# Kernel tuning notes

Measured on AMD Instinct MI355X. Metric: run time of the kernel, lower is better.

The kernel has to match this reference:

```python
import jax, jax.numpy as jnp
import numpy as np

B, N = 2048, 64
D, H = 64, 256
CARD_V, UNIT_V, ENEMY_V, AT_V, SRC_V, MODE_V, TER_V, SITE_V, SKILL_V = 400, 100, 120, 50, 30, 10, 12, 25, 60
STATE_SC, CE_SC, SITE_SC, ME_SC, ACT_SC = 64, 8, 6, 8, 16
L_HAND, L_UNIT, L_CE, L_SK, L_VS, L_ME, L_TGT = 16, 8, 8, 8, 16, 16, 8
STATE_IN = STATE_SC + 6 * D + (D + CE_SC) + (D + SITE_SC) + (D + ME_SC)  # 662
ACT_IN = 7 * D + ACT_SC  # 464


def setup_inputs() -> dict:
    key = jax.random.key(0)
    ks = iter(jax.random.split(key, 64))
    nrm = lambda shape, s=1.0: jax.random.normal(next(ks), shape, jnp.float32) * s
    ri = lambda shape, hi: jax.random.randint(next(ks), shape, 0, hi, jnp.int32)
    return {
        'state_scalars': nrm((B, STATE_SC)),
        'mode_id': ri((B,), MODE_V), 'terrain_id': ri((B,), TER_V), 'site_type_id': ri((B,), SITE_V),
        'hand_ids': ri((B, L_HAND), CARD_V), 'hand_mask': ri((B, L_HAND), 2),
        'unit_ids': ri((B, L_UNIT), UNIT_V), 'unit_mask': ri((B, L_UNIT), 2),
        'combat_enemy_ids': ri((B, L_CE), ENEMY_V), 'combat_enemy_scalars': nrm((B, L_CE, CE_SC)), 'combat_enemy_mask': ri((B, L_CE), 2),
        'skill_ids': ri((B, L_SK), SKILL_V), 'skill_mask': ri((B, L_SK), 2),
        'visible_site_ids': ri((B, L_VS), SITE_V), 'visible_site_scalars': nrm((B, L_VS, SITE_SC)), 'visible_site_mask': ri((B, L_VS), 2),
        'map_enemy_ids': ri((B, L_ME), ENEMY_V), 'map_enemy_scalars': nrm((B, L_ME, ME_SC)), 'map_enemy_mask': ri((B, L_ME), 2),
        'action_ids': ri((B, N, 6), SRC_V),  # SRC_V=30 is min over the 6 id vocabs -> always in range
        'action_scalars': nrm((B, N, ACT_SC)),
        'target_enemy_ids': ri((B, N, L_TGT), ENEMY_V), 'target_mask': ri((B, N, L_TGT), 2),
        'card_emb': nrm((CARD_V, D), 0.05), 'unit_emb': nrm((UNIT_V, D), 0.05), 'enemy_emb': nrm((ENEMY_V, D), 0.05),
        'action_type_emb': nrm((AT_V, D), 0.05), 'source_emb': nrm((SRC_V, D), 0.05), 'mode_emb': nrm((MODE_V, D), 0.05),
        'terrain_emb': nrm((TER_V, D), 0.05), 'site_emb': nrm((SITE_V, D), 0.05), 'skill_emb': nrm((SKILL_V, D), 0.05),
        'map_site_emb': nrm((SITE_V, D), 0.05),
        'W_s': nrm((STATE_IN, H), 0.02), 'b_s': jnp.zeros((H,), jnp.float32),
        'W_a': nrm((ACT_IN, H), 0.02), 'b_a': jnp.zeros((H,), jnp.float32),
        'W1': nrm((2 * H, H), 0.02), 'b1': jnp.zeros((H,), jnp.float32),
        'W2': nrm((H, 1), 0.02), 'b2': jnp.zeros((1,), jnp.float32),
        'W_v': nrm((H, 1), 0.02), 'b_v': jnp.zeros((1,), jnp.float32),
    }


def masked_mean(x, mask):
    # x: [..., L, D'], mask: [..., L] (0/1). Empty list -> zeros (count clamped to 1).
    m = mask.astype(x.dtype)[..., None]
    s = jnp.sum(x * m, axis=-2)
    c = jnp.maximum(jnp.sum(m, axis=-2), 1.0)
    return s / c


def reference(state_scalars, mode_id, terrain_id, site_type_id, hand_ids, hand_mask,
              unit_ids, unit_mask, combat_enemy_ids, combat_enemy_scalars, combat_enemy_mask,
              skill_ids, skill_mask, visible_site_ids, visible_site_scalars, visible_site_mask,
              map_enemy_ids, map_enemy_scalars, map_enemy_mask, action_ids, action_scalars,
              target_enemy_ids, target_mask, card_emb, unit_emb, enemy_emb, action_type_emb,
              source_emb, mode_emb, terrain_emb, site_emb, skill_emb, map_site_emb,
              W_s, b_s, W_a, b_a, W1, b1, W2, b2, W_v, b_v):
    # ---- state encoding (batched version of encode_state) ----
    hand_pool = masked_mean(card_emb[hand_ids], hand_mask)            # [B, D]
    unit_pool = masked_mean(unit_emb[unit_ids], unit_mask)            # [B, D]
    ce = jnp.concatenate([enemy_emb[combat_enemy_ids], combat_enemy_scalars], axis=-1)
    ce_pool = masked_mean(ce, combat_enemy_mask)                      # [B, D+CE_SC]
    skill_pool = masked_mean(skill_emb[skill_ids], skill_mask)        # [B, D]
    vs = jnp.concatenate([map_site_emb[visible_site_ids], visible_site_scalars], axis=-1)
    vs_pool = masked_mean(vs, visible_site_mask)                      # [B, D+SITE_SC]
    me = jnp.concatenate([enemy_emb[map_enemy_ids], map_enemy_scalars], axis=-1)
    me_pool = masked_mean(me, map_enemy_mask)                         # [B, D+ME_SC]
    state_input = jnp.concatenate([
        state_scalars, mode_emb[mode_id], hand_pool, unit_pool,
        terrain_emb[terrain_id], site_emb[site_type_id],
        ce_pool, skill_pool, vs_pool, me_pool], axis=-1)              # [B, 662]
    state_repr = jnp.tanh(state_input @ W_s + b_s)                    # [B, H]
    # ---- action encoding (batched encode_actions) ----
    tgt_pool = masked_mean(enemy_emb[target_enemy_ids], target_mask)  # [B, N, D]
    action_input = jnp.concatenate([
        action_type_emb[action_ids[..., 0]], source_emb[action_ids[..., 1]],
        card_emb[action_ids[..., 2]], unit_emb[action_ids[..., 3]],
        enemy_emb[action_ids[..., 4]], skill_emb[action_ids[..., 5]],
        tgt_pool, action_scalars], axis=-1)                           # [B, N, 464]
    action_reprs = jnp.tanh(action_input @ W_a + b_a)                 # [B, N, H]
    # ---- scoring + value heads ----
    state_b = jnp.broadcast_to(state_repr[:, None, :], (state_repr.shape[0], action_reprs.shape[1], state_repr.shape[1]))
    combined = jnp.concatenate([state_b, action_reprs], axis=-1)      # [B, N, 2H]
    logits = (jnp.tanh(combined @ W1 + b1) @ W2 + b2)[..., 0]         # [B, N]
    value = (state_repr @ W_v + b_v)[..., 0]                          # [B]
    return logits, value
```

## Files before the change

### kernel.cpp

```cpp
#include <hip/hip_runtime.h>
#include <hip/hip_bf16.h>

#define BB 2048
#define NN 64
#define DD 64
#define HH 256
#define L_HAND 16
#define L_UNIT 8
#define L_CE 8
#define L_SK 8
#define L_VS 16
#define L_ME 16
#define L_TGT 8
#define STATE_SC 64
#define CE_SC 8
#define SITE_SC 6
#define ME_SC 8
#define ACT_SC 16
#define STATE_IN 662
#define ACT_IN 464

#define SROWS 2
#define SK 672
#define SSTRIDE 676

typedef __attribute__((ext_vector_type(8))) short short8;
typedef __attribute__((ext_vector_type(4))) float f32x4;

__device__ __forceinline__ float fast_tanh(float x) {
    float e = __expf(2.0f * x);
    return 1.0f - 2.0f * __builtin_amdgcn_rcpf(e + 1.0f);
}
__device__ __forceinline__ short f2bs(float x) {
    __hip_bfloat16 h = __float2bfloat16(x);
    return *reinterpret_cast<short*>(&h);
}
__device__ __forceinline__ float bs2f(short u) {
    union { unsigned int i; float f; } v;
    v.i = ((unsigned int)(unsigned short)u) << 16;
    return v.f;
}
__device__ __forceinline__ void async_copy16(const void* gsrc, void* ldst) {
    __builtin_amdgcn_global_load_lds(
        (const __attribute__((address_space(1))) unsigned int*)gsrc,
        (__attribute__((address_space(3))) unsigned int*)ldst, 16, 0, 0);
}
__device__ __forceinline__ float sum16_dpp(float v) {
    int x;
    x = __builtin_amdgcn_update_dpp(0, __float_as_int(v), 0x111, 0xf, 0xf, true);
    v += __int_as_float(x);
    x = __builtin_amdgcn_update_dpp(0, __float_as_int(v), 0x112, 0xf, 0xf, true);
    v += __int_as_float(x);
    x = __builtin_amdgcn_update_dpp(0, __float_as_int(v), 0x114, 0xf, 0xf, true);
    v += __int_as_float(x);
    x = __builtin_amdgcn_update_dpp(0, __float_as_int(v), 0x118, 0xf, 0xf, true);
    v += __int_as_float(x);
    return v;
}

#define RO_AT    0
#define RO_SRC   50
#define RO_CARD  80
#define RO_UNIT  480
#define RO_ENEMY 580
#define RO_SKILL 700
#define EMB_ROWS 760

#define T0 (480 * 256)
#define T1 (T0 + 256 * 256)
#define T2 (T1 + EMB_ROWS * 64)
#define T3 (T2 + SK * 256)
#define T4 (T3 + 256 * 256)

__global__ __launch_bounds__(256) void pack_kernel(
    const float* __restrict__ W_a, const float* __restrict__ W1,
    const float* __restrict__ W_s,
    const float* __restrict__ at_emb, const float* __restrict__ src_emb,
    const float* __restrict__ card_emb, const float* __restrict__ unit_emb,
    const float* __restrict__ enemy_emb, const float* __restrict__ skill_emb,
    ushort* __restrict__ WaP, ushort* __restrict__ W1bP, ushort* __restrict__ emb16,
    ushort* __restrict__ WsP, ushort* __restrict__ W1aP)
{
    const int idx = blockIdx.x * 256 + threadIdx.x;
    if (idx < T0) {
        const int k = idx >> 8, n = idx & 255;
        const float v = (k < ACT_IN) ? W_a[k * HH + n] : 0.f;
        const int pi = (((k >> 5) * 16 + (n >> 4)) * 64 +
                        ((n & 15) + 16 * ((k >> 3) & 3))) * 8 + (k & 7);
        WaP[pi] = (ushort)f2bs(v);
    } else if (idx < T1) {
        const int j = idx - T0;
        const int k = j >> 8, n = j & 255;
        const float v = W1[(256 + k) * HH + n];
        const int pi = (((k >> 5) * 16 + (n >> 4)) * 64 +
                        ((n & 15) + 16 * ((k >> 3) & 3))) * 8 + (k & 7);
        W1bP[pi] = (ushort)f2bs(v);
    } else if (idx < T2) {
        const int j = idx - T1;
        const int row = j >> 6, d = j & 63;
        float v;
        if      (row < RO_SRC)   v = at_emb[row * 64 + d];
        else if (row < RO_CARD)  v = src_emb[(row - RO_SRC) * 64 + d];
        else if (row < RO_UNIT)  v = card_emb[(row - RO_CARD) * 64 + d];
        else if (row < RO_ENEMY) v = unit_emb[(row - RO_UNIT) * 64 + d];
        else if (row < RO_SKILL) v = enemy_emb[(row - RO_ENEMY) * 64 + d];
        else                     v = skill_emb[(row - RO_SKILL) * 64 + d];
        emb16[j] = (ushort)f2bs(v);
    } else if (idx < T3) {
        const int j = idx - T2;
        const int k = j >> 8, n = j & 255;
        const float v = (k < STATE_IN) ? W_s[k * HH + n] : 0.f;
        const int pi = (((k >> 5) * 16 + (n >> 4)) * 64 +
                        ((n & 15) + 16 * ((k >> 3) & 3))) * 8 + (k & 7);
        WsP[pi] = (ushort)f2bs(v);
    } else if (idx < T4) {
        const int j = idx - T3;
        const int k = j >> 8, n = j & 255;
        const float v = W1[k * HH + n];
        const int pi = (((k >> 5) * 16 + (n >> 4)) * 64 +
                        ((n & 15) + 16 * ((k >> 3) & 3))) * 8 + (k & 7);
        W1aP[pi] = (ushort)f2bs(v);
    }
}

__global__ __launch_bounds__(256) void state_mfma_kernel(
    const float* __restrict__ state_scalars,
    const int* __restrict__ mode_id, const int* __restrict__ terrain_id,
    const int* __restrict__ site_type_id,
    const int* __restrict__ hand_ids, const int* __restrict__ hand_mask,
    const int* __restrict__ unit_ids, const int* __restrict__ unit_mask,
    const int* __restrict__ ce_ids, const float* __restrict__ ce_sc, const int* __restrict__ ce_mask,
    const int* __restrict__ skill_ids, const int* __restrict__ skill_mask,
    const int* __restrict__ vs_ids, const float* __restrict__ vs_sc, const int* __restrict__ vs_mask,
    const int* __restrict__ me_ids, const float* __restrict__ me_sc, const int* __restrict__ me_mask,
    const float* __restrict__ mode_emb, const float* __restrict__ ter_emb,
    const float* __restrict__ site_emb, const float* __restrict__ msite_emb,
    const ushort* __restrict__ emb16,
    const ushort* __restrict__ WsP, const float* __restrict__ b_s,
    const ushort* __restrict__ W1aP,
    const float* __restrict__ W_v, const float* __restrict__ b_v,
    float* __restrict__ s_part, float* __restrict__ out_value)
{
    __shared__ float s_in[SROWS * SSTRIDE];
    __shared__ ushort sA2[8 * 64 * 8];
    __shared__ float red[4][4];

    const int t = threadIdx.x;
    const int b0 = blockIdx.x * SROWS;
    const int w = t >> 6;
    const int lane = t & 63;
    const ushort* card16  = emb16 + RO_CARD  * 64;
    const ushort* unit16  = emb16 + RO_UNIT  * 64;
    const ushort* enemy16 = emb16 + RO_ENEMY * 64;
    const ushort* skill16 = emb16 + RO_SKILL * 64;

    for (int u = t; u < SROWS * 84; u += 256) {
        const int r  = u / 84;
        const int un = u - r * 84;
        const int b  = b0 + r;
        float* dst = s_in + r * SSTRIDE;
        if (un < 8) {
            const int o0 = un * 8;
            const float4 f0 = *(const float4*)(state_scalars + b * STATE_SC + o0);
            const float4 f1 = *(const float4*)(state_scalars + b * STATE_SC + o0 + 4);
            *(float4*)(dst + o0) = f0; *(float4*)(dst + o0 + 4) = f1;
        } else if (un < 16) {
            const int d0 = (un - 8) * 8;
            const float4 f0 = *(const float4*)(mode_emb + mode_id[b] * DD + d0);
            const float4 f1 = *(const float4*)(mode_emb + mode_id[b] * DD + d0 + 4);
            *(float4*)(dst + 64 + d0) = f0; *(float4*)(dst + 64 + d0 + 4) = f1;
        } else if (un < 24) {
            const int d0 = (un - 16) * 8;
            float acc[8] = {0,0,0,0,0,0,0,0}; int c = 0;
#pragma unroll
            for (int l = 0; l < L_HAND; ++l) {
                const int mk = hand_mask[b * L_HAND + l]; c += mk;
                const float fm = (float)mk;
                const short8 e = *(const short8*)(card16 + hand_ids[b * L_HAND + l] * 64 + d0);
#pragma unroll
                for (int q = 0; q < 8; ++q) acc[q] = fmaf(fm, bs2f(e[q]), acc[q]);
            }
            const float inv = 1.0f / (float)(c > 1 ? c : 1);
#pragma unroll
            for (int q = 0; q < 8; ++q) dst[128 + d0 + q] = acc[q] * inv;
        } else if (un < 32) {
            const int d0 = (un - 24) * 8;
            float acc[8] = {0,0,0,0,0,0,0,0}; int c = 0;
#pragma unroll
            for (int l = 0; l < L_UNIT; ++l) {
                const int mk = unit_mask[b * L_UNIT + l]; c += mk;
                const float fm = (float)mk;
                const short8 e = *(const short8*)(unit16 + unit_ids[b * L_UNIT + l] * 64 + d0);
#pragma unroll
                for (int q = 0; q < 8; ++q) acc[q] = fmaf(fm, bs2f(e[q]), acc[q]);
            }
            const float inv = 1.0f / (float)(c > 1 ? c : 1);
#pragma unroll
            for (int q = 0; q < 8; ++q) dst[192 + d0 + q] = acc[q] * inv;
        } else if (un < 40) {
            const int d0 = (un - 32) * 8;
            const float4 f0 = *(const float4*)(ter_emb + terrain_id[b] * DD + d0);
            const float4 f1 = *(const float4*)(ter_emb + terrain_id[b] * DD + d0 + 4);
            *(float4*)(dst + 256 + d0) = f0; *(float4*)(dst + 256 + d0 + 4) = f1;
        } else if (un < 48) {
            const int d0 = (un - 40) * 8;
            const float4 f0 = *(const float4*)(site_emb + site_type_id[b] * DD + d0);
            const float4 f1 = *(const float4*)(site_emb + site_type_id[b] * DD + d0 + 4);
            *(float4*)(dst + 320 + d0) = f0; *(float4*)(dst + 320 + d0 + 4) = f1;
        } else if (un < 56) {
            const int d0 = (un - 48) * 8;
            float acc[8] = {0,0,0,0,0,0,0,0}; int c = 0;
#pragma unroll
            for (int l = 0; l < L_CE; ++l) {
                const int mk = ce_mask[b * L_CE + l]; c += mk;
                const float fm = (float)mk;
                const short8 e = *(const short8*)(enemy16 + ce_ids[b * L_CE + l] * 64 + d0);
#pragma unroll
                for (int q = 0; q < 8; ++q) acc[q] = fmaf(fm, bs2f(e[q]), acc[q]);
            }
            const float inv = 1.0f / (float)(c > 1 ? c : 1);
#pragma unroll
            for (int q = 0; q < 8; ++q) dst[384 + d0 + q] = acc[q] * inv;
        } else if (un == 56) {
            float acc[8] = {0,0,0,0,0,0,0,0}; int c = 0;
#pragma unroll
            for (int l = 0; l < L_CE; ++l) {
                const int mk = ce_mask[b * L_CE + l]; c += mk;
                const float fm = (float)mk;
                const float4 f0 = *(const float4*)(ce_sc + (b * L_CE + l) * CE_SC);
                const float4 f1 = *(const float4*)(ce_sc + (b * L_CE + l) * CE_SC + 4);
                acc[0] = fmaf(fm, f0.x, acc[0]); acc[1] = fmaf(fm, f0.y, acc[1]);
                acc[2] = fmaf(fm, f0.z, acc[2]); acc[3] = fmaf(fm, f0.w, acc[3]);
                acc[4] = fmaf(fm, f1.x, acc[4]); acc[5] = fmaf(fm, f1.y, acc[5]);
                acc[6] = fmaf(fm, f1.z, acc[6]); acc[7] = fmaf(fm, f1.w, acc[7]);
            }
            const float inv = 1.0f / (float)(c > 1 ? c : 1);
#pragma unroll
            for (int q = 0; q < 8; ++q) dst[448 + q] = acc[q] * inv;
        } else if (un < 65) {
            const int d0 = (un - 57) * 8;
            float acc[8] = {0,0,0,0,0,0,0,0}; int c = 0;
#pragma unroll
            for (int l = 0; l < L_SK; ++l) {
                const int mk = skill_mask[b * L_SK + l]; c += mk;
                const float fm = (float)mk;
                const short8 e = *(const short8*)(skill16 + skill_ids[b * L_SK + l] * 64 + d0);
#pragma unroll
                for (int q = 0; q < 8; ++q) acc[q] = fmaf(fm, bs2f(e[q]), acc[q]);
            }
            const float inv = 1.0f / (float)(c > 1 ? c : 1);
#pragma unroll
            for (int q = 0; q < 8; ++q) dst[456 + d0 + q] = acc[q] * inv;
        } else if (un < 73) {
            const int d0 = (un - 65) * 8;
            float acc[8] = {0,0,0,0,0,0,0,0}; int c = 0;
#pragma unroll
            for (int l = 0; l < L_VS; ++l) {
                const int mk = vs_mask[b * L_VS + l]; c += mk;
                const float fm = (float)mk;
                const float4 f0 = *(const float4*)(msite_emb + vs_ids[b * L_VS + l] * DD + d0);
                const float4 f1 = *(const float4*)(msite_emb + vs_ids[b * L_VS + l] * DD + d0 + 4);
                acc[0] = fmaf(fm, f0.x, acc[0]); acc[1] = fmaf(fm, f0.y, acc[1]);
                acc[2] = fmaf(fm, f0.z, acc[2]); acc[3] = fmaf(fm, f0.w, acc[3]);
                acc[4] = fmaf(fm, f1.x, acc[4]); acc[5] = fmaf(fm, f1.y, acc[5]);
                acc[6] = fmaf(fm, f1.z, acc[6]); acc[7] = fmaf(fm, f1.w, acc[7]);
            }
            const float inv = 1.0f / (float)(c > 1 ? c : 1);
#pragma unroll
            for (int q = 0; q < 8; ++q) dst[520 + d0 + q] = acc[q] * inv;
        } else if (un == 73) {
            float acc[6] = {0,0,0,0,0,0}; int c = 0;
#pragma unroll
            for (int l = 0; l < L_VS; ++l) {
                const int mk = vs_mask[b * L_VS + l]; c += mk;
                const float fm = (float)mk;
                const float* p = vs_sc + (b * L_VS + l) * SITE_SC;
#pragma unroll
                for (int q = 0; q < 6; ++q) acc[q] = fmaf(fm, p[q], acc[q]);
            }
            const float inv = 1.0f / (float)(c > 1 ? c : 1);
#pragma unroll
            for (int q = 0; q < 6; ++q) dst[584 + q] = acc[q] * inv;
        } else if (un < 82) {
            const int d0 = (un - 74) * 8;
            float acc[8] = {0,0,0,0,0,0,0,0}; int c = 0;
#pragma unroll
            for (int l = 0; l < L_ME; ++l) {
                const int mk = me_mask[b * L_ME + l]; c += mk;
                const float fm = (float)mk;
                const short8 e = *(const short8*)(enemy16 + me_ids[b * L_ME + l] * 64 + d0);
#pragma unroll
                for (int q = 0; q < 8; ++q) acc[q] = fmaf(fm, bs2f(e[q]), acc[q]);
            }
            const float inv = 1.0f / (float)(c > 1 ? c : 1);
#pragma unroll
            for (int q = 0; q < 8; ++q) dst[590 + d0 + q] = acc[q] * inv;
        } else if (un == 82) {
            float acc[8] = {0,0,0,0,0,0,0,0}; int c = 0;
#pragma unroll
            for (int l = 0; l < L_ME; ++l) {
                const int mk = me_mask[b * L_ME + l]; c += mk;
                const float fm = (float)mk;
                const float4 f0 = *(const float4*)(me_sc + (b * L_ME + l) * ME_SC);
                const float4 f1 = *(const float4*)(me_sc + (b * L_ME + l) * ME_SC + 4);
                acc[0] = fmaf(fm, f0.x, acc[0]); acc[1] = fmaf(fm, f0.y, acc[1]);
                acc[2] = fmaf(fm, f0.z, acc[2]); acc[3] = fmaf(fm, f0.w, acc[3]);
                acc[4] = fmaf(fm, f1.x, acc[4]); acc[5] = fmaf(fm, f1.y, acc[5]);
                acc[6] = fmaf(fm, f1.z, acc[6]); acc[7] = fmaf(fm, f1.w, acc[7]);
            }
            const float inv = 1.0f / (float)(c > 1 ? c : 1);
#pragma unroll
            for (int q = 0; q < 8; ++q) dst[654 + q] = acc[q] * inv;
        } else {
#pragma unroll
            for (int q = 0; q < 10; ++q) dst[662 + q] = 0.f;
        }
    }
    __syncthreads();

    const short8* Ws8  = (const short8*)WsP;
    const short8* W1a8 = (const short8*)W1aP;
    const f32x4 zero = {0.f, 0.f, 0.f, 0.f};
    const int m15 = lane & 15;
    const int g = lane >> 4;
    const float* arow = s_in + (m15 & (SROWS - 1)) * SSTRIDE;

    f32x4 acc1[4];
#pragma unroll
    for (int nt = 0; nt < 4; ++nt) acc1[nt] = zero;

    for (int kt = 0; kt < 21; ++kt) {
        const int k0 = kt * 32 + 8 * g;
        const float4 v0 = *(const float4*)(arow + k0);
        const float4 v1 = *(const float4*)(arow + k0 + 4);
        short8 a;
        a[0] = f2bs(v0.x); a[1] = f2bs(v0.y); a[2] = f2bs(v0.z); a[3] = f2bs(v0.w);
        a[4] = f2bs(v1.x); a[5] = f2bs(v1.y); a[6] = f2bs(v1.z); a[7] = f2bs(v1.w);
        short8 bfr[4];
#pragma unroll
        for (int nt = 0; nt < 4; ++nt) bfr[nt] = Ws8[(kt * 16 + w * 4 + nt) * 64 + lane];
#pragma unroll
        for (int nt = 0; nt < 4; ++nt)
            acc1[nt] = __builtin_amdgcn_mfma_f32_16x16x32_bf16(a, bfr[nt], acc1[nt], 0, 0, 0);
    }

    float sr[4][4];
    float pv[4] = {0.f, 0.f, 0.f, 0.f};
#pragma unroll
    for (int nt = 0; nt < 4; ++nt) {
        const int n = w * 64 + nt * 16 + m15;
        const float bsn = b_s[n];
        const float wvn = W_v[n];
#pragma unroll
        for (int r = 0; r < 4; ++r) {
            const float sv = fast_tanh(acc1[nt][r] + bsn);
            sr[nt][r] = sv;
            pv[r] = fmaf(sv, wvn, pv[r]);
        }
    }
#pragma unroll
    for (int r = 0; r < SROWS; ++r) {
        float v = pv[r];
        v += __shfl_xor(v, 1);
        v += __shfl_xor(v, 2);
        v += __shfl_xor(v, 4);
        v += __shfl_xor(v, 8);
        if (lane == 0) red[w][r] = v;
    }
    if (g == 0) {
#pragma unroll
        for (int nt = 0; nt < 4; ++nt) {
            const int n = w * 64 + nt * 16 + m15;
            const int kt2 = n >> 5;
            const int lo16 = (n >> 3) & 3;
#pragma unroll
            for (int r = 0; r < 4; ++r) {
                const int pi = (kt2 * 64 + (r + 16 * lo16)) * 8 + (n & 7);
                sA2[pi] = (ushort)f2bs(sr[nt][r]);
            }
        }
    }
    __syncthreads();

    if (t < SROWS) {
        out_value[b0 + t] = red[0][t] + red[1][t] + red[2][t] + red[3][t] + b_v[0];
    }

    const short8* sA2_8 = (const short8*)sA2;
    f32x4 acc2[4];
#pragma unroll
    for (int nt = 0; nt < 4; ++nt) acc2[nt] = zero;
#pragma unroll
    for (int kt = 0; kt < 8; ++kt) {
        const short8 a2 = sA2_8[kt * 64 + lane];
        short8 bfr[4];
#pragma unroll
        for (int nt = 0; nt < 4; ++nt) bfr[nt] = W1a8[(kt * 16 + w * 4 + nt) * 64 + lane];
#pragma unroll
        for (int nt = 0; nt < 4; ++nt)
            acc2[nt] = __builtin_amdgcn_mfma_f32_16x16x32_bf16(a2, bfr[nt], acc2[nt], 0, 0, 0);
    }
    if (g == 0) {
#pragma unroll
        for (int nt = 0; nt < 4; ++nt) {
            const int n = w * 64 + nt * 16 + m15;
#pragma unroll
            for (int r = 0; r < SROWS; ++r)
                s_part[(b0 + r) * HH + n] = acc2[nt][r];
        }
    }
}

__device__ __forceinline__ short8 tail_chunk(
    int k0, int m, int b,
    const int* __restrict__ tgt_ids, const int* __restrict__ tgt_mask,
    const ushort* __restrict__ emb16, const float* __restrict__ action_scalars)
{
    short8 val;
    if (k0 < 448) {
        const int d = k0 - 384;
        const ushort* enemy16 = emb16 + RO_ENEMY * 64;
        const int base = (b * NN + m) * L_TGT;
        const int4 t0v = *(const int4*)(tgt_ids + base);
        const int4 t1v = *(const int4*)(tgt_ids + base + 4);
        const int4 m0v = *(const int4*)(tgt_mask + base);
        const int4 m1v = *(const int4*)(tgt_mask + base + 4);
        const int tid[8] = {t0v.x, t0v.y, t0v.z, t0v.w, t1v.x, t1v.y, t1v.z, t1v.w};
        const int tmk[8] = {m0v.x, m0v.y, m0v.z, m0v.w, m1v.x, m1v.y, m1v.z, m1v.w};
        float accq[8] = {0.f, 0.f, 0.f, 0.f, 0.f, 0.f, 0.f, 0.f};
        int c = 0;
#pragma unroll
        for (int l = 0; l < L_TGT; ++l) {
            const int mk = tmk[l];
            c += mk;
            const float fm = (float)mk;
            const short8 e = *(const short8*)(enemy16 + tid[l] * 64 + d);
#pragma unroll
            for (int q = 0; q < 8; ++q) accq[q] = fmaf(fm, bs2f(e[q]), accq[q]);
        }
        const float inv = 1.0f / (float)(c > 1 ? c : 1);
#pragma unroll
        for (int q = 0; q < 8; ++q) val[q] = f2bs(accq[q] * inv);
    } else if (k0 < 464) {
        const float* sc = action_scalars + (b * NN + m) * ACT_SC + (k0 - 448);
        const float4 f0 = *(const float4*)sc;
        const float4 f1 = *(const float4*)(sc + 4);
        val[0] = f2bs(f0.x); val[1] = f2bs(f0.y); val[2] = f2bs(f0.z); val[3] = f2bs(f0.w);
        val[4] = f2bs(f1.x); val[5] = f2bs(f1.y); val[6] = f2bs(f1.z); val[7] = f2bs(f1.w);
    } else {
#pragma unroll
        for (int q = 0; q < 8; ++q) val[q] = 0;
    }
    return val;
}

__global__ __launch_bounds__(512) void action_mfma_kernel(
    const int* __restrict__ action_ids, const float* __restrict__ action_scalars,
    const int* __restrict__ tgt_ids, const int* __restrict__ tgt_mask,
    const ushort* __restrict__ emb16,
    const ushort* __restrict__ WaP, const float* __restrict__ b_a,
    const ushort* __restrict__ W1bP, const float* __restrict__ b1,
    const float* __restrict__ W2, const float* __restrict__ b2,
    const float* __restrict__ s_part, float* __restrict__ out_logits)
{
    __shared__ ushort sA[15 * 2048];
    __shared__ float red[8][64];

    const int t = threadIdx.x;
    const int b = blockIdx.x;
    const int w = t >> 6;
    const int lane = t & 63;
    const int m15 = lane & 15;

    const short8* sA8  = (const short8*)sA;
    short8* sA8w = (short8*)sA;
    const short8* Wa8  = (const short8*)WaP;
    const short8* W1b8 = (const short8*)W1bP;
    const f32x4 zero = {0.f, 0.f, 0.f, 0.f};
    const int* aid = action_ids + b * (NN * 6);

    short8 bp00 = Wa8[(0 * 16 + w * 2 + 0) * 64 + lane];
    short8 bp01 = Wa8[(0 * 16 + w * 2 + 1) * 64 + lane];
    short8 bp10 = Wa8[(1 * 16 + w * 2 + 0) * 64 + lane];
    short8 bp11 = Wa8[(1 * 16 + w * 2 + 1) * 64 + lane];

    const int ROFFS[6] = {RO_AT, RO_SRC, RO_CARD, RO_UNIT, RO_ENEMY, RO_SKILL};

    {
        const int kt = w;
        const int j = kt >> 1;
        const int roff = ROFFS[j];
        const int koff = (kt & 1) * 32 + (lane >> 4) * 8;
#pragma unroll
        for (int i = 0; i < 4; ++i) {
            const int id = aid[(i * 16 + m15) * 6 + j];
            async_copy16(emb16 + (roff + id) * 64 + koff, sA + kt * 2048 + i * 512);
        }
    }
    if (w < 4) {
        const int kt = 8 + w;
        const int j = kt >> 1;
        const int roff = ROFFS[j];
        const int koff = (kt & 1) * 32 + (lane >> 4) * 8;
#pragma unroll
        for (int i = 0; i < 4; ++i) {
            const int id = aid[(i * 16 + m15) * 6 + j];
            async_copy16(emb16 + (roff + id) * 64 + koff, sA + kt * 2048 + i * 512);
        }
    }

    {
        const int m = lane;
        const int mt_b = m >> 4, mrow = m & 15;
        for (int kc = 48 + w; kc < 60; kc += 8) {
            const int k0 = kc << 3;
            const short8 val = tail_chunk(k0, m, b, tgt_ids, tgt_mask, emb16, action_scalars);
            const int ktl = k0 >> 5;
            const int lo = kc & 3;
            sA8w[(ktl * 4 + mt_b) * 64 + mrow + 16 * lo] = val;
        }
    }
    __syncthreads();

    float ba[2];
#pragma unroll
    for (int nt = 0; nt < 2; ++nt) ba[nt] = b_a[w * 32 + nt * 16 + m15];

    f32x4 acc[4][2];
#pragma unroll
    for (int i = 0; i < 4; ++i) { acc[i][0] = zero; acc[i][1] = zero; }

#pragma unroll
    for (int kt = 0; kt < 15; ++kt) {
        short8 b0, b1;
        if ((kt & 1) == 0) { b0 = bp00; b1 = bp01; }
        else               { b0 = bp10; b1 = bp11; }
        if (kt + 2 < 15) {
            if ((kt & 1) == 0) {
                bp00 = Wa8[((kt + 2) * 16 + w * 2 + 0) * 64 + lane];
                bp01 = Wa8[((kt + 2) * 16 + w * 2 + 1) * 64 + lane];
            } else {
                bp10 = Wa8[((kt + 2) * 16 + w * 2 + 0) * 64 + lane];
                bp11 = Wa8[((kt + 2) * 16 + w * 2 + 1) * 64 + lane];
            }
        } else if (kt + 2 == 15) {
            bp10 = W1b8[(0 * 16 + w * 2 + 0) * 64 + lane];
            bp11 = W1b8[(0 * 16 + w * 2 + 1) * 64 + lane];
        } else {
            bp00 = W1b8[(1 * 16 + w * 2 + 0) * 64 + lane];
            bp01 = W1b8[(1 * 16 + w * 2 + 1) * 64 + lane];
        }
        short8 a[4];
#pragma unroll
        for (int mti = 0; mti < 4; ++mti) a[mti] = sA8[(kt * 4 + mti) * 64 + lane];
#pragma unroll
        for (int mti = 0; mti < 4; ++mti) {
            acc[mti][0] = __builtin_amdgcn_mfma_f32_16x16x32_bf16(a[mti], b0, acc[mti][0], 0, 0, 0);
            acc[mti][1] = __builtin_amdgcn_mfma_f32_16x16x32_bf16(a[mti], b1, acc[mti][1], 0, 0, 0);
        }
    }
    __syncthreads();

#pragma unroll
    for (int mti = 0; mti < 4; ++mti)
#pragma unroll
        for (int nt = 0; nt < 2; ++nt) {
            const int n = w * 32 + nt * 16 + m15;
            const int kt2 = n >> 5;
            const int lo16 = (n >> 3) & 3;
#pragma unroll
            for (int r = 0; r < 4; ++r) {
                const int mm = mti * 16 + (lane >> 4) * 4 + r;
                const float h = fast_tanh(acc[mti][nt][r] + ba[nt]);
                const int pi = ((kt2 * 4 + mti) * 64 + ((mm & 15) + 16 * lo16)) * 8 + (n & 7);
                sA[pi] = (ushort)f2bs(h);
            }
        }
    __syncthreads();

    float sp[2], w2v[2];
#pragma unroll
    for (int nt = 0; nt < 2; ++nt) {
        const int n = w * 32 + nt * 16 + m15;
        sp[nt]  = s_part[b * HH + n] + b1[n];
        w2v[nt] = W2[n];
    }

#pragma unroll
    for (int i = 0; i < 4; ++i) { acc[i][0] = zero; acc[i][1] = zero; }

#pragma unroll
    for (int kt = 0; kt < 8; ++kt) {
        short8 b0, b1;
        if ((kt & 1) == 0) { b0 = bp10; b1 = bp11; }
        else               { b0 = bp00; b1 = bp01; }
        if (kt + 2 < 8) {
            if ((kt & 1) == 0) {
                bp10 = W1b8[((kt + 2) * 16 + w * 2 + 0) * 64 + lane];
                bp11 = W1b8[((kt + 2) * 16 + w * 2 + 1) * 64 + lane];
            } else {
                bp00 = W1b8[((kt + 2) * 16 + w * 2 + 0) * 64 + lane];
                bp01 = W1b8[((kt + 2) * 16 + w * 2 + 1) * 64 + lane];
            }
        }
        short8 a[4];
#pragma unroll
        for (int mti = 0; mti < 4; ++mti) a[mti] = sA8[(kt * 4 + mti) * 64 + lane];
#pragma unroll
        for (int mti = 0; mti < 4; ++mti) {
            acc[mti][0] = __builtin_amdgcn_mfma_f32_16x16x32_bf16(a[mti], b0, acc[mti][0], 0, 0, 0);
            acc[mti][1] = __builtin_amdgcn_mfma_f32_16x16x32_bf16(a[mti], b1, acc[mti][1], 0, 0, 0);
        }
    }

    float part[4][4];
#pragma unroll
    for (int mti = 0; mti < 4; ++mti)
#pragma unroll
        for (int r = 0; r < 4; ++r) part[mti][r] = 0.f;

#pragma unroll
    for (int mti = 0; mti < 4; ++mti)
#pragma unroll
        for (int nt = 0; nt < 2; ++nt)
#pragma unroll
            for (int r = 0; r < 4; ++r)
                part[mti][r] += fast_tanh(acc[mti][nt][r] + sp[nt]) * w2v[nt];

#pragma unroll
    for (int mti = 0; mti < 4; ++mti)
#pragma unroll
        for (int r = 0; r < 4; ++r)
            part[mti][r] = sum16_dpp(part[mti][r]);

    if (m15 == 15) {
#pragma unroll
        for (int mti = 0; mti < 4; ++mti)
#pragma unroll
            for (int r = 0; r < 4; ++r) {
                const int mm = mti * 16 + (lane >> 4) * 4 + r;
                red[w][mm] = part[mti][r];
            }
    }
    __syncthreads();
    if (t < 64) {
        float s = b2[0];
#pragma unroll
        for (int wi = 0; wi < 8; ++wi) s += red[wi][t];
        out_logits[b * NN + t] = s;
    }
}

extern "C" void kernel_launch(void* const* d_in, const int* in_sizes, int n_in,
                              void* d_out, int out_size, void* d_ws, size_t ws_size,
                              hipStream_t stream) {
    const float* state_scalars = (const float*)d_in[0];
    const int*   mode_id       = (const int*)d_in[1];
    const int*   terrain_id    = (const int*)d_in[2];
    const int*   site_type_id  = (const int*)d_in[3];
    const int*   hand_ids      = (const int*)d_in[4];
    const int*   hand_mask     = (const int*)d_in[5];
    const int*   unit_ids      = (const int*)d_in[6];
    const int*   unit_mask     = (const int*)d_in[7];
    const int*   ce_ids        = (const int*)d_in[8];
    const float* ce_sc         = (const float*)d_in[9];
    const int*   ce_mask       = (const int*)d_in[10];
    const int*   skill_ids     = (const int*)d_in[11];
    const int*   skill_mask    = (const int*)d_in[12];
    const int*   vs_ids        = (const int*)d_in[13];
    const float* vs_sc         = (const float*)d_in[14];
    const int*   vs_mask       = (const int*)d_in[15];
    const int*   me_ids        = (const int*)d_in[16];
    const float* me_sc         = (const float*)d_in[17];
    const int*   me_mask       = (const int*)d_in[18];
    const int*   action_ids    = (const int*)d_in[19];
    const float* action_scalars= (const float*)d_in[20];
    const int*   tgt_ids       = (const int*)d_in[21];
    const int*   tgt_mask      = (const int*)d_in[22];
    const float* card_emb      = (const float*)d_in[23];
    const float* unit_emb      = (const float*)d_in[24];
    const float* enemy_emb     = (const float*)d_in[25];
    const float* at_emb        = (const float*)d_in[26];
    const float* src_emb       = (const float*)d_in[27];
    const float* mode_emb      = (const float*)d_in[28];
    const float* ter_emb       = (const float*)d_in[29];
    const float* site_emb      = (const float*)d_in[30];
    const float* skill_emb     = (const float*)d_in[31];
    const float* msite_emb     = (const float*)d_in[32];
    const float* W_s           = (const float*)d_in[33];
    const float* b_s           = (const float*)d_in[34];
    const float* W_a           = (const float*)d_in[35];
    const float* b_a           = (const float*)d_in[36];
    const float* W1            = (const float*)d_in[37];
    const float* b1            = (const float*)d_in[38];
    const float* W2            = (const float*)d_in[39];
    const float* b2            = (const float*)d_in[40];
    const float* W_v           = (const float*)d_in[41];
    const float* b_v           = (const float*)d_in[42];

    float* out_logits = (float*)d_out;
    float* out_value  = (float*)d_out + (size_t)BB * NN;

    char* ws = (char*)d_ws;
    float*  s_part = (float*)ws;
    ushort* WaP    = (ushort*)(ws + 2097152);
    ushort* W1bP   = (ushort*)(ws + 2342912);
    ushort* emb16  = (ushort*)(ws + 2473984);
    ushort* WsP    = (ushort*)(ws + 2571264);
    ushort* W1aP   = (ushort*)(ws + 2915328);

    pack_kernel<<<(T4 + 255) / 256, 256, 0, stream>>>(
        W_a, W1, W_s, at_emb, src_emb, card_emb, unit_emb, enemy_emb, skill_emb,
        WaP, W1bP, emb16, WsP, W1aP);

    state_mfma_kernel<<<BB / SROWS, 256, 0, stream>>>(
        state_scalars, mode_id, terrain_id, site_type_id,
        hand_ids, hand_mask, unit_ids, unit_mask,
        ce_ids, ce_sc, ce_mask, skill_ids, skill_mask,
        vs_ids, vs_sc, vs_mask, me_ids, me_sc, me_mask,
        mode_emb, ter_emb, site_emb, msite_emb, emb16,
        WsP, b_s, W1aP, W_v, b_v, s_part, out_value);

    action_mfma_kernel<<<BB, 512, 0, stream>>>(
        action_ids, action_scalars, tgt_ids, tgt_mask,
        emb16, WaP, b_a, W1bP, b1, W2, b2, s_part, out_logits);
}
```

Baseline: 111.0 us.

## Make action kernel persistent over batch rows with double-buffered async staging

Each block of the action kernel now processes 8 batch rows instead of one, and launches BB/8 blocks. While row i is being computed, the embedding gather and tail staging for row i+1 go into a second LDS buffer via async global-to-LDS copies. Weight prefetch depth grows from 2 to 4 k-tiles, and barriers become explicit waitcnt plus s_barrier. This should hide gather latency and amortise per-block setup, but it doubles LDS use, which can cut occupancy. Only 256 blocks are launched, so CU utilisation may also drop.

New measurement: 137.3 us. 1.24x slower.

```diff
diff --git a/kernel.cpp b/kernel.cpp
--- a/kernel.cpp
+++ b/kernel.cpp
@@ -23,6 +23,7 @@
 #define SROWS 2
 #define SK 672
 #define SSTRIDE 676
+#define RPB 8
 
 typedef __attribute__((ext_vector_type(8))) short short8;
 typedef __attribute__((ext_vector_type(4))) float f32x4;
@@ -57,6 +58,12 @@
     v += __int_as_float(x);
     return v;
 }
+
+#define LGKM0()  asm volatile("s_waitcnt lgkmcnt(0)" ::: "memory")
+#define VMLG0()  asm volatile("s_waitcnt vmcnt(0) lgkmcnt(0)" ::: "memory")
+#define RAWBAR() do { __builtin_amdgcn_sched_barrier(0); \
+                      __builtin_amdgcn_s_barrier();       \
+                      __builtin_amdgcn_sched_barrier(0); } while (0)
 
 #define RO_AT    0
 #define RO_SRC   50
@@ -463,191 +470,192 @@
     const float* __restrict__ W2, const float* __restrict__ b2,
     const float* __restrict__ s_part, float* __restrict__ out_logits)
 {
-    __shared__ ushort sA[15 * 2048];
+    __shared__ ushort sA[2][15 * 2048];
     __shared__ float red[8][64];
 
     const int t = threadIdx.x;
-    const int b = blockIdx.x;
     const int w = t >> 6;
     const int lane = t & 63;
     const int m15 = lane & 15;
-
-    const short8* sA8  = (const short8*)sA;
-    short8* sA8w = (short8*)sA;
+    const int b_base = blockIdx.x * RPB;
+
     const short8* Wa8  = (const short8*)WaP;
     const short8* W1b8 = (const short8*)W1bP;
     const f32x4 zero = {0.f, 0.f, 0.f, 0.f};
-    const int* aid = action_ids + b * (NN * 6);
-
-    short8 bp00 = Wa8[(0 * 16 + w * 2 + 0) * 64 + lane];
-    short8 bp01 = Wa8[(0 * 16 + w * 2 + 1) * 64 + lane];
-    short8 bp10 = Wa8[(1 * 16 + w * 2 + 0) * 64 + lane];
-    short8 bp11 = Wa8[(1 * 16 + w * 2 + 1) * 64 + lane];
-
     const int ROFFS[6] = {RO_AT, RO_SRC, RO_CARD, RO_UNIT, RO_ENEMY, RO_SKILL};
 
-    {
-        const int kt = w;
-        const int j = kt >> 1;
-        const int roff = ROFFS[j];
-        const int koff = (kt & 1) * 32 + (lane >> 4) * 8;
-#pragma unroll
-        for (int i = 0; i < 4; ++i) {
-            const int id = aid[(i * 16 + m15) * 6 + j];
-            async_copy16(emb16 + (roff + id) * 64 + koff, sA + kt * 2048 + i * 512);
-        }
-    }
-    if (w < 4) {
-        const int kt = 8 + w;
-        const int j = kt >> 1;
-        const int roff = ROFFS[j];
-        const int koff = (kt & 1) * 32 + (lane >> 4) * 8;
-#pragma unroll
-        for (int i = 0; i < 4; ++i) {
-            const int id = aid[(i * 16 + m15) * 6 + j];
-            async_copy16(emb16 + (roff + id) * 64 + koff, sA + kt * 2048 + i * 512);
-        }
-    }
-
-    {
-        const int m = lane;
-        const int mt_b = m >> 4, mrow = m & 15;
+    float ba[2], w2v[2], b1v[2];
+#pragma unroll
+    for (int nt = 0; nt < 2; ++nt) {
+        const int n = w * 32 + nt * 16 + m15;
+        ba[nt]  = b_a[n];
+        w2v[nt] = W2[n];
+        b1v[nt] = b1[n];
+    }
+    const float b2v = b2[0];
+
+    auto STAGE = [&](int b, ushort* sbuf) {
+        const int* aid = action_ids + b * (NN * 6);
+        {
+            const int kt = w;
+            const int j = kt >> 1;
+            const int roff = ROFFS[j];
+            const int koff = (kt & 1) * 32 + (lane >> 4) * 8;
+#pragma unroll
+            for (int i = 0; i < 4; ++i) {
+                const int id = aid[(i * 16 + m15) * 6 + j];
+                async_copy16(emb16 + (roff + id) * 64 + koff, sbuf + kt * 2048 + i * 512);
+            }
+        }
+        if (w < 4) {
+            const int kt = 8 + w;
+            const int j = kt >> 1;
+            const int roff = ROFFS[j];
+            const int koff = (kt & 1) * 32 + (lane >> 4) * 8;
+#pragma unroll
+            for (int i = 0; i < 4; ++i) {
+                const int id = aid[(i * 16 + m15) * 6 + j];
+                async_copy16(emb16 + (roff + id) * 64 + koff, sbuf + kt * 2048 + i * 512);
+            }
+        }
+        short8* s8 = (short8*)sbuf;
+        const int m = lane, mt_b = m >> 4, mrow = m & 15;
         for (int kc = 48 + w; kc < 60; kc += 8) {
             const int k0 = kc << 3;
             const short8 val = tail_chunk(k0, m, b, tgt_ids, tgt_mask, emb16, action_scalars);
-            const int ktl = k0 >> 5;
-            const int lo = kc & 3;
-            sA8w[(ktl * 4 + mt_b) * 64 + mrow + 16 * lo] = val;
-        }
-    }
-    __syncthreads();
-
-    float ba[2];
-#pragma unroll
-    for (int nt = 0; nt < 2; ++nt) ba[nt] = b_a[w * 32 + nt * 16 + m15];
-
-    f32x4 acc[4][2];
-#pragma unroll
-    for (int i = 0; i < 4; ++i) { acc[i][0] = zero; acc[i][1] = zero; }
-
-#pragma unroll
-    for (int kt = 0; kt < 15; ++kt) {
-        short8 b0, b1;
-        if ((kt & 1) == 0) { b0 = bp00; b1 = bp01; }
-        else               { b0 = bp10; b1 = bp11; }
-        if (kt + 2 < 15) {
-            if ((kt & 1) == 0) {
-                bp00 = Wa8[((kt + 2) * 16 + w * 2 + 0) * 64 + lane];
-                bp01 = Wa8[((kt + 2) * 16 + w * 2 + 1) * 64 + lane];
+            s8[((k0 >> 5) * 4 + mt_b) * 64 + mrow + 16 * (kc & 3)] = val;
+        }
+    };
+
+    STAGE(b_base, &sA[0][0]);
+    VMLG0();
+    RAWBAR();
+
+    for (int i = 0; i < RPB; ++i) {
+        const int b = b_base + i;
+        const short8* cur = (const short8*)&sA[i & 1][0];
+        ushort* curw = &sA[i & 1][0];
+
+        if (i + 1 < RPB) STAGE(b + 1, &sA[(i + 1) & 1][0]);
+
+        short8 bq[4][2];
+#pragma unroll
+        for (int p = 0; p < 4; ++p) {
+            bq[p][0] = Wa8[(p * 16 + w * 2 + 0) * 64 + lane];
+            bq[p][1] = Wa8[(p * 16 + w * 2 + 1) * 64 + lane];
+        }
+
+        f32x4 acc[4][2];
+#pragma unroll
+        for (int x = 0; x < 4; ++x) { acc[x][0] = zero; acc[x][1] = zero; }
+
+#pragma unroll
+        for (int kt = 0; kt < 15; ++kt) {
+            const int s = kt & 3;
+            const short8 bf0 = bq[s][0], bf1 = bq[s][1];
+            if (kt + 4 < 15) {
+                bq[s][0] = Wa8[((kt + 4) * 16 + w * 2 + 0) * 64 + lane];
+                bq[s][1] = Wa8[((kt + 4) * 16 + w * 2 + 1) * 64 + lane];
             } else {
-                bp10 = Wa8[((kt + 2) * 16 + w * 2 + 0) * 64 + lane];
-                bp11 = Wa8[((kt + 2) * 16 + w * 2 + 1) * 64 + lane];
-            }
-        } else if (kt + 2 == 15) {
-            bp10 = W1b8[(0 * 16 + w * 2 + 0) * 64 + lane];
-            bp11 = W1b8[(0 * 16 + w * 2 + 1) * 64 + lane];
-        } else {
-            bp00 = W1b8[(1 * 16 + w * 2 + 0) * 64 + lane];
-            bp01 = W1b8[(1 * 16 + w * 2 + 1) * 64 + lane];
-        }
-        short8 a[4];
-#pragma unroll
-        for (int mti = 0; mti < 4; ++mti) a[mti] = sA8[(kt * 4 + mti) * 64 + lane];
-#pragma unroll
-        for (int mti = 0; mti < 4; ++mti) {
-            acc[mti][0] = __builtin_amdgcn_mfma_f32_16x16x32_bf16(a[mti], b0, acc[mti][0], 0, 0, 0);
-            acc[mti][1] = __builtin_amdgcn_mfma_f32_16x16x32_bf16(a[mti], b1, acc[mti][1], 0, 0, 0);
-        }
-    }
-    __syncthreads();
-
-#pragma unroll
-    for (int mti = 0; mti < 4; ++mti)
-#pragma unroll
-        for (int nt = 0; nt < 2; ++nt) {
-            const int n = w * 32 + nt * 16 + m15;
-            const int kt2 = n >> 5;
-            const int lo16 = (n >> 3) & 3;
-#pragma unroll
-            for (int r = 0; r < 4; ++r) {
-                const int mm = mti * 16 + (lane >> 4) * 4 + r;
-                const float h = fast_tanh(acc[mti][nt][r] + ba[nt]);
-                const int pi = ((kt2 * 4 + mti) * 64 + ((mm & 15) + 16 * lo16)) * 8 + (n & 7);
-                sA[pi] = (ushort)f2bs(h);
-            }
-        }
-    __syncthreads();
-
-    float sp[2], w2v[2];
-#pragma unroll
-    for (int nt = 0; nt < 2; ++nt) {
-        const int n = w * 32 + nt * 16 + m15;
-        sp[nt]  = s_part[b * HH + n] + b1[n];
-        w2v[nt] = W2[n];
-    }
-
-#pragma unroll
-    for (int i = 0; i < 4; ++i) { acc[i][0] = zero; acc[i][1] = zero; }
-
-#pragma unroll
-    for (int kt = 0; kt < 8; ++kt) {
-        short8 b0, b1;
-        if ((kt & 1) == 0) { b0 = bp10; b1 = bp11; }
-        else               { b0 = bp00; b1 = bp01; }
-        if (kt + 2 < 8) {
-            if ((kt & 1) == 0) {
-                bp10 = W1b8[((kt + 2) * 16 + w * 2 + 0) * 64 + lane];
-                bp11 = W1b8[((kt + 2) * 16 + w * 2 + 1) * 64 + lane];
-            } else {
-                bp00 = W1b8[((kt + 2) * 16 + w * 2 + 0) * 64 + lane];
-                bp01 = W1b8[((kt + 2) * 16 + w * 2 + 1) * 64 + lane];
-            }
-        }
-        short8 a[4];
-#pragma unroll
-        for (int mti = 0; mti < 4; ++mti) a[mti] = sA8[(kt * 4 + mti) * 64 + lane];
-#pragma unroll
-        for (int mti = 0; mti < 4; ++mti) {
-            acc[mti][0] = __builtin_amdgcn_mfma_f32_16x16x32_bf16(a[mti], b0, acc[mti][0], 0, 0, 0);
-            acc[mti][1] = __builtin_amdgcn_mfma_f32_16x16x32_bf16(a[mti], b1, acc[mti][1], 0, 0, 0);
-        }
-    }
-
-    float part[4][4];
-#pragma unroll
-    for (int mti = 0; mti < 4; ++mti)
-#pragma unroll
-        for (int r = 0; r < 4; ++r) part[mti][r] = 0.f;
-
-#pragma unroll
-    for (int mti = 0; mti < 4; ++mti)
+                const int g2 = kt - 11;
+                bq[s][0] = W1b8[(g2 * 16 + w * 2 + 0) * 64 + lane];
+                bq[s][1] = W1b8[(g2 * 16 + w * 2 + 1) * 64 + lane];
+            }
+            short8 a[4];
+#pragma unroll
+            for (int mti = 0; mti < 4; ++mti) a[mti] = cur[(kt * 4 + mti) * 64 + lane];
+#pragma unroll
+            for (int mti = 0; mti < 4; ++mti) {
+                acc[mti][0] = __builtin_amdgcn_mfma_f32_16x16x32_bf16(a[mti], bf0, acc[mti][0], 0, 0, 0);
+                acc[mti][1] = __builtin_amdgcn_mfma_f32_16x16x32_bf16(a[mti], bf1, acc[mti][1], 0, 0, 0);
+            }
+        }
+        LGKM0();
+        RAWBAR();
+
+#pragma unroll
+        for (int mti = 0; mti < 4; ++mti)
+#pragma unroll
+            for (int nt = 0; nt < 2; ++nt) {
+                const int n = w * 32 + nt * 16 + m15;
+                const int kt2 = n >> 5;
+                const int lo16 = (n >> 3) & 3;
+#pragma unroll
+                for (int r = 0; r < 4; ++r) {
+                    const int mm = mti * 16 + (lane >> 4) * 4 + r;
+                    const float h = fast_tanh(acc[mti][nt][r] + ba[nt]);
+                    const int pi = ((kt2 * 4 + mti) * 64 + ((mm & 15) + 16 * lo16)) * 8 + (n & 7);
+                    curw[pi] = (ushort)f2bs(h);
+                }
+            }
+        float sp[2];
 #pragma unroll
         for (int nt = 0; nt < 2; ++nt)
+            sp[nt] = s_part[b * HH + (w * 32 + nt * 16 + m15)] + b1v[nt];
+
+        LGKM0();
+        RAWBAR();
+
+#pragma unroll
+        for (int x = 0; x < 4; ++x) { acc[x][0] = zero; acc[x][1] = zero; }
+
+#pragma unroll
+        for (int kt = 0; kt < 8; ++kt) {
+            const int s = (kt + 3) & 3;
+            const short8 bf0 = bq[s][0], bf1 = bq[s][1];
+            if (kt + 4 < 8) {
+                bq[s][0] = W1b8[((kt + 4) * 16 + w * 2 + 0) * 64 + lane];
+                bq[s][1] = W1b8[((kt + 4) * 16 + w * 2 + 1) * 64 + lane];
+            }
+            short8 a[4];
+#pragma unroll
+            for (int mti = 0; mti < 4; ++mti) a[mti] = cur[(kt * 4 + mti) * 64 + lane];
+#pragma unroll
+            for (int mti = 0; mti < 4; ++mti) {
+                acc[mti][0] = __builtin_amdgcn_mfma_f32_16x16x32_bf16(a[mti], bf0, acc[mti][0], 0, 0, 0);
+                acc[mti][1] = __builtin_amdgcn_mfma_f32_16x16x32_bf16(a[mti], bf1, acc[mti][1], 0, 0, 0);
+            }
+        }
+
+        float part[4][4];
+#pragma unroll
+        for (int mti = 0; mti < 4; ++mti)
+#pragma unroll
+            for (int r = 0; r < 4; ++r) part[mti][r] = 0.f;
+
+#pragma unroll
+        for (int mti = 0; mti < 4; ++mti)
+#pragma unroll
+            for (int nt = 0; nt < 2; ++nt)
+#pragma unroll
+                for (int r = 0; r < 4; ++r)
+                    part[mti][r] += fast_tanh(acc[mti][nt][r] + sp[nt]) * w2v[nt];
+
+#pragma unroll
+        for (int mti = 0; mti < 4; ++mti)
 #pragma unroll
             for (int r = 0; r < 4; ++r)
-                part[mti][r] += fast_tanh(acc[mti][nt][r] + sp[nt]) * w2v[nt];
-
-#pragma unroll
-    for (int mti = 0; mti < 4; ++mti)
-#pragma unroll
-        for (int r = 0; r < 4; ++r)
-            part[mti][r] = sum16_dpp(part[mti][r]);
-
-    if (m15 == 15) {
-#pragma unroll
-        for (int mti = 0; mti < 4; ++mti)
-#pragma unroll
-            for (int r = 0; r < 4; ++r) {
-                const int mm = mti * 16 + (lane >> 4) * 4 + r;
-                red[w][mm] = part[mti][r];
-            }
-    }
-    __syncthreads();
-    if (t < 64) {
-        float s = b2[0];
-#pragma unroll
-        for (int wi = 0; wi < 8; ++wi) s += red[wi][t];
-        out_logits[b * NN + t] = s;
+                part[mti][r] = sum16_dpp(part[mti][r]);
+
+        if (m15 == 15) {
+#pragma unroll
+            for (int mti = 0; mti < 4; ++mti)
+#pragma unroll
+                for (int r = 0; r < 4; ++r) {
+                    const int mm = mti * 16 + (lane >> 4) * 4 + r;
+                    red[w][mm] = part[mti][r];
+                }
+        }
+
+        VMLG0();
+        RAWBAR();
+
+        if (t < 64) {
+            float s = b2v;
+#pragma unroll
+            for (int wi = 0; wi < 8; ++wi) s += red[wi][t];
+            out_logits[b * NN + t] = s;
+        }
     }
 }
 
@@ -721,7 +729,7 @@
         mode_emb, ter_emb, site_emb, msite_emb, emb16,
         WsP, b_s, W1aP, W_v, b_v, s_part, out_value);
 
-    action_mfma_kernel<<<BB, 512, 0, stream>>>(
+    action_mfma_kernel<<<BB / RPB, 512, 0, stream>>>(
         action_ids, action_scalars, tgt_ids, tgt_mask,
         emb16, WaP, b_a, W1bP, b1, W2, b2, s_part, out_logits);
 }
```
